# Kernel tuning notes

Hardware: AMD Instinct MI355X
Metric: run time of the kernel (lower is better)

The kernel has to match this reference:

```python
import jax, jax.numpy as jnp
import numpy as np

N = 50000
E = 800000
DIMS = [(8, 16), (16, 16), (16, 16)]  # (in, out) per layer


def setup_inputs() -> dict:
    key = jax.random.key(0)
    ks = jax.random.split(key, 32)
    inp = {}
    inp['x'] = jax.random.normal(ks[0], (N, 8), dtype=jnp.float32)
    inp['pos'] = jax.random.normal(ks[1], (N, 3), dtype=jnp.float32)
    k = 2
    for i, (ci, co) in enumerate(DIMS):
        d = ci * co
        inp[f'lin_w{i}'] = jax.random.normal(ks[k], (3, d), dtype=jnp.float32); k += 1
        inp[f'lin_b{i}'] = jax.random.normal(ks[k], (d,), dtype=jnp.float32); k += 1
        inp[f'gamma{i}'] = jax.random.normal(ks[k], (d,), dtype=jnp.float32); k += 1
        inp[f'beta{i}'] = jax.random.normal(ks[k], (d,), dtype=jnp.float32); k += 1
        inp[f'root{i}'] = jax.random.normal(ks[k], (ci, co), dtype=jnp.float32); k += 1
        inp[f'bias{i}'] = jax.random.normal(ks[k], (co,), dtype=jnp.float32); k += 1
    inp['batch'] = jnp.zeros((N,), dtype=jnp.int32)
    inp['idx'] = jnp.sort(jax.random.randint(ks[k], (25000,), 0, N, dtype=jnp.int32)); k += 1
    inp['edge_index'] = jax.random.randint(ks[k], (2, E), 0, N, dtype=jnp.int32)
    return inp


def _nnconv(x, pseudo, src, dst, lin_w, lin_b, gamma, beta, root, bias, ci, co):
    # edge MLP (Linear -> batchnorm(eval, affine) -> ReLU), plain_last=False
    w = jax.nn.relu((pseudo @ lin_w + lin_b) * gamma + beta)  # [E, ci*co]
    w = w.reshape(-1, ci, co)                                  # [E, ci, co]
    msg = jnp.einsum('ei,eio->eo', x[src], w)                  # per-edge vec-mat
    s = jax.ops.segment_sum(msg, dst, num_segments=N)          # scatter-sum
    cnt = jax.ops.segment_sum(jnp.ones((msg.shape[0],), x.dtype), dst, num_segments=N)
    aggr = s / jnp.maximum(cnt, 1.0)[:, None]                  # scatter-mean
    return aggr + x @ root + bias


def reference(x, pos, lin_w0, lin_b0, gamma0, beta0, root0, bias0,
              lin_w1, lin_b1, gamma1, beta1, root1, bias1,
              lin_w2, lin_b2, gamma2, beta2, root2, bias2,
              batch, idx, edge_index):
    src, dst = edge_index[0], edge_index[1]
    pseudo = pos[dst] - pos[src]  # patch_size is None
    params = [
        (lin_w0, lin_b0, gamma0, beta0, root0, bias0),
        (lin_w1, lin_b1, gamma1, beta1, root1, bias1),
        (lin_w2, lin_b2, gamma2, beta2, root2, bias2),
    ]
    h = x
    for (ci, co), p in zip(DIMS, params):
        h = jax.nn.relu(_nnconv(h, pseudo, src, dst, *p, ci, co))  # drop_act=False
    return h[idx], pos[idx], batch[idx]
```

## Files before the change

### kernel.cpp

```cpp
#include <hip/hip_runtime.h>

#define N_NODES 50000
#define N_EDGES 800000
#define M_IDX   25000
#define DMAX    64

__global__ __launch_bounds__(256) void prep_kernel(
    const int*   __restrict__ ei,
    const float* __restrict__ pos,
    int*         __restrict__ cnt,
    float4*      __restrict__ pdata,
    int E)
{
    const int e0 = blockIdx.x * 512 + threadIdx.x;
    const int e1 = e0 + 256;
    const bool v0 = e0 < E, v1 = e1 < E;
    int t0 = 0, s0 = 0, t1 = 0, s1 = 0;
    if (v0) { t0 = ei[E + e0]; s0 = ei[e0]; }
    if (v1) { t1 = ei[E + e1]; s1 = ei[e1]; }
    int p0 = 0, p1 = 0;
    if (v0) p0 = atomicAdd(&cnt[t0], 1);
    if (v1) p1 = atomicAdd(&cnt[t1], 1);
    if (v0) {
        float4 pd;
        pd.x = pos[t0 * 3 + 0] - pos[s0 * 3 + 0];
        pd.y = pos[t0 * 3 + 1] - pos[s0 * 3 + 1];
        pd.z = pos[t0 * 3 + 2] - pos[s0 * 3 + 2];
        pd.w = __int_as_float(s0);
        if (p0 < DMAX) pdata[(size_t)t0 * DMAX + p0] = pd;
    }
    if (v1) {
        float4 pd;
        pd.x = pos[t1 * 3 + 0] - pos[s1 * 3 + 0];
        pd.y = pos[t1 * 3 + 1] - pos[s1 * 3 + 1];
        pd.z = pos[t1 * 3 + 2] - pos[s1 * 3 + 2];
        pd.w = __int_as_float(s1);
        if (p1 < DMAX) pdata[(size_t)t1 * DMAX + p1] = pd;
    }
}

template<int CI>
__global__ __launch_bounds__(256) void node_wave_kernel(
    const float4* __restrict__ pdata,
    const int*    __restrict__ cnt,
    const float*  __restrict__ h_in,
    const float*  __restrict__ lin_w,
    const float*  __restrict__ lin_b,
    const float*  __restrict__ gamma,
    const float*  __restrict__ beta,
    const float*  __restrict__ root,
    const float*  __restrict__ bias,
    float*        __restrict__ h_out,
    int N)
{
    __shared__ float4 wlds[CI * 16];

    const int tid = threadIdx.x;
    if (tid < CI * 16) {
        const int j = tid;
        const float g = gamma[j];
        float4 w4;
        w4.x = lin_w[j] * g;
        w4.y = lin_w[CI * 16 + j] * g;
        w4.z = lin_w[2 * CI * 16 + j] * g;
        w4.w = fmaf(lin_b[j], g, beta[j]);
        wlds[j] = w4;
    }
    __syncthreads();

    const int lane = tid & 63;
    const int eg   = lane >> 4;
    const int o    = lane & 15;
    const int t    = blockIdx.x * 4 + (tid >> 6);

    const int deg = cnt[t];
    const int dl  = min(deg, DMAX);
    const float4* __restrict__ row = pdata + (size_t)t * DMAX;

    float acc = 0.f;
    for (int p = eg; p < dl; p += 8) {
        const int  p1 = p + 4;
        const bool v1 = p1 < dl;
        float4 pdA = row[p];
        float4 pdB = v1 ? row[p1] : pdA;
        const float4* xa = (const float4*)(h_in + (size_t)__float_as_int(pdA.w) * CI);
        const float4* xb = (const float4*)(h_in + (size_t)__float_as_int(pdB.w) * CI);
        float xA[CI], xB[CI];
#pragma unroll
        for (int q = 0; q < CI / 4; ++q) {
            float4 a = xa[q];
            xA[4 * q + 0] = a.x; xA[4 * q + 1] = a.y;
            xA[4 * q + 2] = a.z; xA[4 * q + 3] = a.w;
            float4 b = xb[q];
            xB[4 * q + 0] = b.x; xB[4 * q + 1] = b.y;
            xB[4 * q + 2] = b.z; xB[4 * q + 3] = b.w;
        }
        float eA = 0.f, eB = 0.f;
#pragma unroll
        for (int i = 0; i < CI; ++i) {
            float4 w4 = wlds[i * 16 + o];
            float wA = fmaf(pdA.z, w4.z, fmaf(pdA.y, w4.y, fmaf(pdA.x, w4.x, w4.w)));
            eA = fmaf(xA[i], fmaxf(wA, 0.f), eA);
            float wB = fmaf(pdB.z, w4.z, fmaf(pdB.y, w4.y, fmaf(pdB.x, w4.x, w4.w)));
            eB = fmaf(xB[i], fmaxf(wB, 0.f), eB);
        }
        acc += eA + (v1 ? eB : 0.f);
    }
    acc += __shfl_xor(acc, 16);
    acc += __shfl_xor(acc, 32);

    float r = fmaf(acc, 1.0f / fmaxf((float)deg, 1.0f), bias[o]);
    const float4* hp = (const float4*)(h_in + (size_t)t * CI);
#pragma unroll
    for (int q = 0; q < CI / 4; ++q) {
        float4 v = hp[q];
        r = fmaf(v.x, root[(4 * q + 0) * 16 + o], r);
        r = fmaf(v.y, root[(4 * q + 1) * 16 + o], r);
        r = fmaf(v.z, root[(4 * q + 2) * 16 + o], r);
        r = fmaf(v.w, root[(4 * q + 3) * 16 + o], r);
    }
    if (eg == 0) h_out[t * 16 + o] = fmaxf(r, 0.f);
}

__global__ __launch_bounds__(256) void gather_kernel(
    const float* __restrict__ h,
    const float* __restrict__ pos,
    const int*   __restrict__ batch,
    const int*   __restrict__ idx,
    float*       __restrict__ out,
    int M)
{
    int j = blockIdx.x * blockDim.x + threadIdx.x;
    if (j >= M) return;
    int n = idx[j];
    float4*       o4 = (float4*)out + (size_t)j * 4;
    const float4* h4 = (const float4*)(h + (size_t)n * 16);
    o4[0] = h4[0]; o4[1] = h4[1]; o4[2] = h4[2]; o4[3] = h4[3];
    float* po = out + (size_t)M * 16 + (size_t)j * 3;
    po[0] = pos[n * 3 + 0];
    po[1] = pos[n * 3 + 1];
    po[2] = pos[n * 3 + 2];
    ((int*)out)[(size_t)M * 19 + j] = batch[n];
}

extern "C" void kernel_launch(void* const* d_in, const int* in_sizes, int n_in,
                              void* d_out, int out_size, void* d_ws, size_t ws_size,
                              hipStream_t stream) {
    const float* x      = (const float*)d_in[0];
    const float* pos    = (const float*)d_in[1];
    const float* lin_w0 = (const float*)d_in[2];
    const float* lin_b0 = (const float*)d_in[3];
    const float* gamma0 = (const float*)d_in[4];
    const float* beta0  = (const float*)d_in[5];
    const float* root0  = (const float*)d_in[6];
    const float* bias0  = (const float*)d_in[7];
    const float* lin_w1 = (const float*)d_in[8];
    const float* lin_b1 = (const float*)d_in[9];
    const float* gamma1 = (const float*)d_in[10];
    const float* beta1  = (const float*)d_in[11];
    const float* root1  = (const float*)d_in[12];
    const float* bias1  = (const float*)d_in[13];
    const float* lin_w2 = (const float*)d_in[14];
    const float* lin_b2 = (const float*)d_in[15];
    const float* gamma2 = (const float*)d_in[16];
    const float* beta2  = (const float*)d_in[17];
    const float* root2  = (const float*)d_in[18];
    const float* bias2  = (const float*)d_in[19];
    const int*   batch  = (const int*)d_in[20];
    const int*   idx    = (const int*)d_in[21];
    const int*   ei     = (const int*)d_in[22];
    float*       out    = (float*)d_out;

    float4* pdata = (float4*)d_ws;
    float*  hA    = (float*)(pdata + (size_t)N_NODES * DMAX);
    float*  hB    = hA + (size_t)N_NODES * 16;
    int*    cnt   = (int*)(hB + (size_t)N_NODES * 16);

    hipMemsetAsync(cnt, 0, N_NODES * sizeof(int), stream);
    prep_kernel<<<(N_EDGES + 511) / 512, 256, 0, stream>>>(ei, pos, cnt, pdata, N_EDGES);

    const int NB = N_NODES / 4;

    node_wave_kernel<8><<<NB, 256, 0, stream>>>(pdata, cnt, x,
        lin_w0, lin_b0, gamma0, beta0, root0, bias0, hA, N_NODES);
    node_wave_kernel<16><<<NB, 256, 0, stream>>>(pdata, cnt, hA,
        lin_w1, lin_b1, gamma1, beta1, root1, bias1, hB, N_NODES);
    node_wave_kernel<16><<<NB, 256, 0, stream>>>(pdata, cnt, hB,
        lin_w2, lin_b2, gamma2, beta2, root2, bias2, hA, N_NODES);

    gather_kernel<<<(M_IDX + 255) / 256, 256, 0, stream>>>(hA, pos, batch, idx, out, M_IDX);
}
```

Baseline: 350.5 us.

## Split input channels across lane groups instead of edges in node kernel

The node kernel now gives each 16-lane group a quarter of the input channels for every edge, where before each group took a quarter of the edges. Each lane keeps its slice of the folded edge-MLP weights in registers, which removes the shared-memory table and the block barrier. Per-lane work per edge drops to CI/4 channels, but every group now walks all edges, so the edge record loads are replicated four times. The root matmul is split the same way and reduced with the existing shuffles.

```diff
diff --git a/kernel.cpp b/kernel.cpp
--- a/kernel.cpp
+++ b/kernel.cpp
@@ -39,6 +39,17 @@
     }
 }
 
+template<int IQ>
+__device__ __forceinline__ void load_q(float* dst, const float* src) {
+    if constexpr (IQ == 4) {
+        float4 v = *(const float4*)src;
+        dst[0] = v.x; dst[1] = v.y; dst[2] = v.z; dst[3] = v.w;
+    } else {
+        float2 v = *(const float2*)src;
+        dst[0] = v.x; dst[1] = v.y;
+    }
+}
+
 template<int CI>
 __global__ __launch_bounds__(256) void node_wave_kernel(
     const float4* __restrict__ pdata,
@@ -53,73 +64,73 @@
     float*        __restrict__ h_out,
     int N)
 {
-    __shared__ float4 wlds[CI * 16];
-
-    const int tid = threadIdx.x;
-    if (tid < CI * 16) {
-        const int j = tid;
-        const float g = gamma[j];
-        float4 w4;
-        w4.x = lin_w[j] * g;
-        w4.y = lin_w[CI * 16 + j] * g;
-        w4.z = lin_w[2 * CI * 16 + j] * g;
-        w4.w = fmaf(lin_b[j], g, beta[j]);
-        wlds[j] = w4;
-    }
-    __syncthreads();
-
+    constexpr int IQ = CI / 4;
+    const int tid  = threadIdx.x;
     const int lane = tid & 63;
     const int eg   = lane >> 4;
     const int o    = lane & 15;
     const int t    = blockIdx.x * 4 + (tid >> 6);
 
+    float W0[IQ], W1[IQ], W2[IQ], B[IQ];
+#pragma unroll
+    for (int z = 0; z < IQ; ++z) {
+        const int j = (eg * IQ + z) * 16 + o;
+        const float g = gamma[j];
+        W0[z] = lin_w[j] * g;
+        W1[z] = lin_w[CI * 16 + j] * g;
+        W2[z] = lin_w[2 * CI * 16 + j] * g;
+        B[z]  = fmaf(lin_b[j], g, beta[j]);
+    }
+
     const int deg = cnt[t];
     const int dl  = min(deg, DMAX);
     const float4* __restrict__ row = pdata + (size_t)t * DMAX;
+    const float*  __restrict__ xq_base = h_in + eg * IQ;
 
     float acc = 0.f;
-    for (int p = eg; p < dl; p += 8) {
-        const int  p1 = p + 4;
-        const bool v1 = p1 < dl;
+    int p = 0;
+    for (; p + 2 <= dl; p += 2) {
         float4 pdA = row[p];
-        float4 pdB = v1 ? row[p1] : pdA;
-        const float4* xa = (const float4*)(h_in + (size_t)__float_as_int(pdA.w) * CI);
-        const float4* xb = (const float4*)(h_in + (size_t)__float_as_int(pdB.w) * CI);
-        float xA[CI], xB[CI];
-#pragma unroll
-        for (int q = 0; q < CI / 4; ++q) {
-            float4 a = xa[q];
-            xA[4 * q + 0] = a.x; xA[4 * q + 1] = a.y;
-            xA[4 * q + 2] = a.z; xA[4 * q + 3] = a.w;
-            float4 b = xb[q];
-            xB[4 * q + 0] = b.x; xB[4 * q + 1] = b.y;
-            xB[4 * q + 2] = b.z; xB[4 * q + 3] = b.w;
+        float4 pdB = row[p + 1];
+        const int sA = __float_as_int(pdA.w);
+        const int sB = __float_as_int(pdB.w);
+        float xA[IQ], xB[IQ];
+        load_q<IQ>(xA, xq_base + (size_t)sA * CI);
+        load_q<IQ>(xB, xq_base + (size_t)sB * CI);
+        float eA = 0.f, eB = 0.f;
+#pragma unroll
+        for (int z = 0; z < IQ; ++z) {
+            float wA = fmaf(pdA.z, W2[z], fmaf(pdA.y, W1[z], fmaf(pdA.x, W0[z], B[z])));
+            eA = fmaf(xA[z], fmaxf(wA, 0.f), eA);
+            float wB = fmaf(pdB.z, W2[z], fmaf(pdB.y, W1[z], fmaf(pdB.x, W0[z], B[z])));
+            eB = fmaf(xB[z], fmaxf(wB, 0.f), eB);
         }
-        float eA = 0.f, eB = 0.f;
-#pragma unroll
-        for (int i = 0; i < CI; ++i) {
-            float4 w4 = wlds[i * 16 + o];
-            float wA = fmaf(pdA.z, w4.z, fmaf(pdA.y, w4.y, fmaf(pdA.x, w4.x, w4.w)));
-            eA = fmaf(xA[i], fmaxf(wA, 0.f), eA);
-            float wB = fmaf(pdB.z, w4.z, fmaf(pdB.y, w4.y, fmaf(pdB.x, w4.x, w4.w)));
-            eB = fmaf(xB[i], fmaxf(wB, 0.f), eB);
+        acc += eA + eB;
+    }
+    if (p < dl) {
+        float4 pdA = row[p];
+        const int sA = __float_as_int(pdA.w);
+        float xA[IQ];
+        load_q<IQ>(xA, xq_base + (size_t)sA * CI);
+#pragma unroll
+        for (int z = 0; z < IQ; ++z) {
+            float wA = fmaf(pdA.z, W2[z], fmaf(pdA.y, W1[z], fmaf(pdA.x, W0[z], B[z])));
+            acc = fmaf(xA[z], fmaxf(wA, 0.f), acc);
         }
-        acc += eA + (v1 ? eB : 0.f);
-    }
-    acc += __shfl_xor(acc, 16);
-    acc += __shfl_xor(acc, 32);
-
-    float r = fmaf(acc, 1.0f / fmaxf((float)deg, 1.0f), bias[o]);
-    const float4* hp = (const float4*)(h_in + (size_t)t * CI);
-#pragma unroll
-    for (int q = 0; q < CI / 4; ++q) {
-        float4 v = hp[q];
-        r = fmaf(v.x, root[(4 * q + 0) * 16 + o], r);
-        r = fmaf(v.y, root[(4 * q + 1) * 16 + o], r);
-        r = fmaf(v.z, root[(4 * q + 2) * 16 + o], r);
-        r = fmaf(v.w, root[(4 * q + 3) * 16 + o], r);
-    }
-    if (eg == 0) h_out[t * 16 + o] = fmaxf(r, 0.f);
+    }
+
+    float xT[IQ];
+    load_q<IQ>(xT, xq_base + (size_t)t * CI);
+    float rp = 0.f;
+#pragma unroll
+    for (int z = 0; z < IQ; ++z)
+        rp = fmaf(xT[z], root[(eg * IQ + z) * 16 + o], rp);
+
+    float contrib = fmaf(acc, 1.0f / fmaxf((float)deg, 1.0f), rp);
+    contrib += __shfl_xor(contrib, 16);
+    contrib += __shfl_xor(contrib, 32);
+
+    if (eg == 0) h_out[t * 16 + o] = fmaxf(contrib + bias[o], 0.f);
 }
 
 __global__ __launch_bounds__(256) void gather_kernel(
```

After: 337.1 us. 3.8% less time.
